# Optimization experiments

Measured on AMD Instinct MI355X. Metric: run time of the kernel, lower is better.

## Reference

```python
import jax, jax.numpy as jnp
import numpy as np

# Circuit structure constants (match init_kwargs)
N_NODES = 32768        # number of sum nodes in this layer
N_CHILD = 65536        # number of child nodes
NNZ = 1048576          # number of sparse weight entries (avg fan-in 32)
BATCH = 128


def setup_inputs() -> dict:
    key = jax.random.key(0)
    k1, k2, k3, k4 = jax.random.split(key, 4)
    # child log-likelihoods per sample (output of child layers)
    child_ll = jax.random.normal(k1, (BATCH, N_CHILD), dtype=jnp.float32)
    # sparse log-weights of the BCOO weight matrix [N_NODES, N_CHILD]
    log_w = jax.random.normal(k2, (NNZ,), dtype=jnp.float32)
    rows = jnp.sort(jax.random.randint(k3, (NNZ,), 0, N_NODES)).astype(jnp.int64)
    cols = jax.random.randint(k4, (NNZ,), 0, N_CHILD).astype(jnp.int64)
    return {"child_ll": child_ll, "log_w": log_w, "rows": rows, "cols": cols}


def reference(child_ll, log_w, rows, cols):
    """Faithful jax translation of SumLayer.log_likelihood_of_nodes.

    Original: per sample, exponentiate BCOO log-weights and child
    log-likelihoods, sparse matvec (weights @ exp(child_ll)), then
    log(result) - log_normalization_constants, where the normalization
    constants are log(row-sums of exp(log_weights)).
    """
    w = jnp.exp(log_w)  # [NNZ]
    # log normalization constants: log of row-sums of exp(log_weights)
    log_z = jnp.log(jax.ops.segment_sum(w, rows, num_segments=N_NODES))  # [N_NODES]

    def per_sample(ll):  # ll: [N_CHILD]
        p = jnp.exp(ll)
        contrib = w * p[cols]                                   # gather + weight [NNZ]
        return jax.ops.segment_sum(contrib, rows, num_segments=N_NODES)  # [N_NODES]

    s = jax.vmap(per_sample)(child_ll)  # [BATCH, N_NODES]
    return jnp.log(s) - log_z
```

## Files before the change

kernel.cpp:

```cpp
#include <hip/hip_runtime.h>
#include <math.h>

#define BATCH     128
#define N_NODES   32768
#define N_CHILD   65536
#define NNZ_TOTAL 1048576
#define LOG2E     1.44269504f

typedef __attribute__((ext_vector_type(2))) float fx2;

__global__ __launch_bounds__(256) void exp8_kernel(
    const float* __restrict__ child_ll, unsigned char* __restrict__ ex8,
    float* __restrict__ winv) {
    const int c0 = blockIdx.x * 64;
    const int t  = threadIdx.x;
    const int cl = t & 63;
    const int q  = t >> 6;

    float v[32];
    float m = -3.4e38f;
    const float* bp = child_ll + (size_t)(q * 32) * N_CHILD + c0 + cl;
#pragma unroll
    for (int j = 0; j < 32; ++j) {
        v[j] = bp[(size_t)j * N_CHILD];
        m = fmaxf(m, v[j]);
    }

    __shared__ float smx[4][64];
    __shared__ float skf[64];
    smx[q][cl] = m;
    __syncthreads();
    if (t < 64) {
        const float mm = fmaxf(fmaxf(smx[0][t], smx[1][t]),
                               fmaxf(smx[2][t], smx[3][t]));
        const int ks = 7 - (int)floorf(mm * LOG2E);
        skf[t] = (float)ks;
        winv[c0 + t] = exp2f((float)(-ks));
    }
    __syncthreads();
    const float kf = skf[cl];

    unsigned ow[8];
#pragma unroll
    for (int p = 0; p < 8; ++p) {
        const float a0 = exp2f(fmaf(v[4 * p + 0], LOG2E, kf));
        const float a1 = exp2f(fmaf(v[4 * p + 1], LOG2E, kf));
        const float a2 = exp2f(fmaf(v[4 * p + 2], LOG2E, kf));
        const float a3 = exp2f(fmaf(v[4 * p + 3], LOG2E, kf));
        unsigned u = 0;
        u = __builtin_amdgcn_cvt_pk_fp8_f32(a0, a1, u, false);
        u = __builtin_amdgcn_cvt_pk_fp8_f32(a2, a3, u, true);
        ow[p] = u;
    }

    __shared__ unsigned char sby[64 * 144];
    *(uint4*)&sby[cl * 144 + q * 32]      = *(uint4*)&ow[0];
    *(uint4*)&sby[cl * 144 + q * 32 + 16] = *(uint4*)&ow[4];
    __syncthreads();

    const int sub = t & 7, cc = t >> 3;
#pragma unroll
    for (int p = 0; p < 2; ++p) {
        const int c = cc + p * 32;
        *(uint4*)&ex8[(size_t)(c0 + c) * 128 + sub * 16] =
            *(const uint4*)&sby[c * 144 + sub * 16];
    }
}

__global__ __launch_bounds__(256) void fold_scan_kernel(
    const float* __restrict__ log_w, const int* __restrict__ cols,
    const float* __restrict__ winv, const int* __restrict__ rows,
    float* __restrict__ wfold, int* __restrict__ row_start) {
    const int i = (blockIdx.x * 256 + threadIdx.x) * 4;
    const float4 lw = *(const float4*)&log_w[i];
    const int4   cc = *(const int4*)&cols[i];
    float4 o;
    o.x = expf(lw.x) * winv[cc.x];
    o.y = expf(lw.y) * winv[cc.y];
    o.z = expf(lw.z) * winv[cc.z];
    o.w = expf(lw.w) * winv[cc.w];
    *(float4*)&wfold[i] = o;

    const int4 rv = *(const int4*)&rows[i];
    const int rj[4] = {rv.x, rv.y, rv.z, rv.w};
    int prev = (i == 0) ? -1 : rows[i - 1];
#pragma unroll
    for (int j = 0; j < 4; ++j) {
        const int cur = rj[j];
        if (cur != prev)
            for (int q = prev + 1; q <= cur; ++q) row_start[q] = i + j;
        prev = cur;
    }
    if (i + 3 == NNZ_TOTAL - 1)
        for (int q = rj[3] + 1; q <= N_NODES; ++q) row_start[q] = NNZ_TOTAL;
}

__global__ __launch_bounds__(256) void logz_kernel(
    const float* __restrict__ log_w, const int* __restrict__ row_start,
    float* __restrict__ logzv) {
    const int t = threadIdx.x;
    const int g = t >> 4, j = t & 15;
    const int r = blockIdx.x * 16 + g;
    const int s = row_start[r], e = row_start[r + 1];
    float sum = 0.f;
    for (int i = s + j; i < e; i += 16) sum += expf(log_w[i]);
    sum += __shfl_xor(sum, 1, 64);
    sum += __shfl_xor(sum, 2, 64);
    sum += __shfl_xor(sum, 4, 64);
    sum += __shfl_xor(sum, 8, 64);
    if (j == 0) logzv[r] = logf(sum);
}

__global__ __launch_bounds__(256, 4) void sum_rows_kernel(
    const unsigned char* __restrict__ ex8, const float* __restrict__ wfold,
    const int* __restrict__ cols, const int* __restrict__ row_start,
    const float* __restrict__ logzv, float* __restrict__ out) {
    const int wave = threadIdx.x >> 6;
    const int lane = threadIdx.x & 63;
    const int bid  = blockIdx.x;
    const int rb   = (bid & 7) * (N_NODES / 4 / 8) + (bid >> 3);
    const int r    = rb * 4 + wave;

    const int start = row_start[r];
    const int end   = row_start[r + 1];
    const int  slot = lane >> 3;
    const unsigned sub = (unsigned)lane & 7u;
    const unsigned boff = sub * 16u;

    float acc[16];
#pragma unroll
    for (int k = 0; k < 16; ++k) acc[k] = 0.f;

    for (int base = start; base < end; base += 64) {
        const int  idx   = base + lane;
        const bool valid = idx < end;
        const int   c  = __builtin_nontemporal_load(&cols[valid ? idx : start]);
        const float wf = valid ? __builtin_nontemporal_load(&wfold[idx]) : 0.f;
        const int seg = end - base;

        int   ct[8];
        float wt[8];
        uint4 g[8];

#pragma unroll
        for (int t8 = 0; t8 < 8; ++t8) {
            if (t8 * 8 < seg) {
                const int pa = (t8 * 8 + slot) * 4;
                ct[t8] = __builtin_amdgcn_ds_bpermute(pa, c);
                wt[t8] = __uint_as_float(__builtin_amdgcn_ds_bpermute(
                    pa, __float_as_uint(wf)));
            }
        }
#pragma unroll
        for (int t8 = 0; t8 < 8; ++t8) {
            if (t8 * 8 < seg)
                g[t8] = *(const uint4*)(ex8 +
                        ((size_t)(unsigned)ct[t8] << 7) + boff);
        }
#pragma unroll
        for (int t8 = 0; t8 < 8; ++t8) {
            if (t8 * 8 < seg) {
                const float wtv = wt[t8];
                const unsigned* gu = (const unsigned*)&g[t8];
#pragma unroll
                for (int q = 0; q < 4; ++q) {
                    const fx2 lo = __builtin_amdgcn_cvt_pk_f32_fp8((int)gu[q], false);
                    const fx2 hi = __builtin_amdgcn_cvt_pk_f32_fp8((int)gu[q], true);
                    acc[q * 4 + 0] = fmaf(wtv, lo.x, acc[q * 4 + 0]);
                    acc[q * 4 + 1] = fmaf(wtv, lo.y, acc[q * 4 + 1]);
                    acc[q * 4 + 2] = fmaf(wtv, hi.x, acc[q * 4 + 2]);
                    acc[q * 4 + 3] = fmaf(wtv, hi.y, acc[q * 4 + 3]);
                }
            }
        }
    }

#pragma unroll
    for (int k = 0; k < 16; ++k) {
        acc[k] += __shfl_xor(acc[k], 8, 64);
        acc[k] += __shfl_xor(acc[k], 16, 64);
        acc[k] += __shfl_xor(acc[k], 32, 64);
    }

    if (lane < 8) {
        const float lz = logzv[r];
        const int b0 = lane * 16;
#pragma unroll
        for (int k = 0; k < 16; ++k)
            out[(size_t)(b0 + k) * N_NODES + r] = logf(acc[k]) - lz;
    }
}

extern "C" void kernel_launch(void* const* d_in, const int* in_sizes, int n_in,
                              void* d_out, int out_size, void* d_ws, size_t ws_size,
                              hipStream_t stream) {
    const float* child_ll = (const float*)d_in[0];
    const float* log_w    = (const float*)d_in[1];
    const int*   rows     = (const int*)d_in[2];
    const int*   cols     = (const int*)d_in[3];
    float*       out      = (float*)d_out;

    unsigned char* ex8 = (unsigned char*)d_ws;
    float* winv      = (float*)((char*)d_ws + (size_t)N_CHILD * 128);
    float* wfold     = (float*)((char*)winv + (size_t)N_CHILD * 4);
    int*   row_start = (int*)((char*)wfold + (size_t)NNZ_TOTAL * 4);
    float* logzv     = (float*)((char*)row_start + (size_t)(N_NODES + 1) * 4);

    exp8_kernel<<<N_CHILD / 64, 256, 0, stream>>>(child_ll, ex8, winv);
    fold_scan_kernel<<<NNZ_TOTAL / 1024, 256, 0, stream>>>(
        log_w, cols, winv, rows, wfold, row_start);
    logz_kernel<<<N_NODES / 16, 256, 0, stream>>>(log_w, row_start, logzv);
    sum_rows_kernel<<<N_NODES / 4, 256, 0, stream>>>(ex8, wfold, cols,
                                                     row_start, logzv, out);
}
```

Baseline: 62.45 us.

## Fold row normalization sums into scan kernel via atomics and spread output stores

Removes the separate logz kernel. Row sums of exp(log_w) are now accumulated with atomicAdd in fold_scan_kernel, and the zeroing of those sums is folded into exp8_kernel. The final log and store in sum_rows_kernel are spread over all 64 lanes, each writing two outputs, instead of 8 lanes writing 16 each. This saves one launch and one reread of log_w, in exchange for atomic traffic and a float summation order that is no longer deterministic.

```diff
diff --git a/kernel.cpp b/kernel.cpp
--- a/kernel.cpp
+++ b/kernel.cpp
@@ -11,9 +11,12 @@
 
 __global__ __launch_bounds__(256) void exp8_kernel(
     const float* __restrict__ child_ll, unsigned char* __restrict__ ex8,
-    float* __restrict__ winv) {
+    float* __restrict__ winv, float* __restrict__ zsum) {
     const int c0 = blockIdx.x * 64;
     const int t  = threadIdx.x;
+    const int gid = blockIdx.x * 256 + t;
+    if (gid < N_NODES) zsum[gid] = 0.f;
+
     const int cl = t & 63;
     const int q  = t >> 6;
 
@@ -70,19 +73,32 @@
 __global__ __launch_bounds__(256) void fold_scan_kernel(
     const float* __restrict__ log_w, const int* __restrict__ cols,
     const float* __restrict__ winv, const int* __restrict__ rows,
-    float* __restrict__ wfold, int* __restrict__ row_start) {
+    float* __restrict__ wfold, int* __restrict__ row_start,
+    float* __restrict__ zsum) {
     const int i = (blockIdx.x * 256 + threadIdx.x) * 4;
     const float4 lw = *(const float4*)&log_w[i];
     const int4   cc = *(const int4*)&cols[i];
+    const float ew0 = expf(lw.x), ew1 = expf(lw.y);
+    const float ew2 = expf(lw.z), ew3 = expf(lw.w);
     float4 o;
-    o.x = expf(lw.x) * winv[cc.x];
-    o.y = expf(lw.y) * winv[cc.y];
-    o.z = expf(lw.z) * winv[cc.z];
-    o.w = expf(lw.w) * winv[cc.w];
+    o.x = ew0 * winv[cc.x];
+    o.y = ew1 * winv[cc.y];
+    o.z = ew2 * winv[cc.z];
+    o.w = ew3 * winv[cc.w];
     *(float4*)&wfold[i] = o;
 
     const int4 rv = *(const int4*)&rows[i];
     const int rj[4] = {rv.x, rv.y, rv.z, rv.w};
+    const float ej[4] = {ew0, ew1, ew2, ew3};
+
+    float s = ej[0];
+#pragma unroll
+    for (int j = 1; j < 4; ++j) {
+        if (rj[j] == rj[j - 1]) s += ej[j];
+        else { atomicAdd(&zsum[rj[j - 1]], s); s = ej[j]; }
+    }
+    atomicAdd(&zsum[rj[3]], s);
+
     int prev = (i == 0) ? -1 : rows[i - 1];
 #pragma unroll
     for (int j = 0; j < 4; ++j) {
@@ -95,26 +111,10 @@
         for (int q = rj[3] + 1; q <= N_NODES; ++q) row_start[q] = NNZ_TOTAL;
 }
 
-__global__ __launch_bounds__(256) void logz_kernel(
-    const float* __restrict__ log_w, const int* __restrict__ row_start,
-    float* __restrict__ logzv) {
-    const int t = threadIdx.x;
-    const int g = t >> 4, j = t & 15;
-    const int r = blockIdx.x * 16 + g;
-    const int s = row_start[r], e = row_start[r + 1];
-    float sum = 0.f;
-    for (int i = s + j; i < e; i += 16) sum += expf(log_w[i]);
-    sum += __shfl_xor(sum, 1, 64);
-    sum += __shfl_xor(sum, 2, 64);
-    sum += __shfl_xor(sum, 4, 64);
-    sum += __shfl_xor(sum, 8, 64);
-    if (j == 0) logzv[r] = logf(sum);
-}
-
 __global__ __launch_bounds__(256, 4) void sum_rows_kernel(
     const unsigned char* __restrict__ ex8, const float* __restrict__ wfold,
     const int* __restrict__ cols, const int* __restrict__ row_start,
-    const float* __restrict__ logzv, float* __restrict__ out) {
+    const float* __restrict__ zsum, float* __restrict__ out) {
     const int wave = threadIdx.x >> 6;
     const int lane = threadIdx.x & 63;
     const int bid  = blockIdx.x;
@@ -123,6 +123,7 @@
 
     const int start = row_start[r];
     const int end   = row_start[r + 1];
+    const float zs  = zsum[r];
     const int  slot = lane >> 3;
     const unsigned sub = (unsigned)lane & 7u;
     const unsigned boff = sub * 16u;
@@ -182,13 +183,17 @@
         acc[k] += __shfl_xor(acc[k], 32, 64);
     }
 
-    if (lane < 8) {
-        const float lz = logzv[r];
-        const int b0 = lane * 16;
-#pragma unroll
-        for (int k = 0; k < 16; ++k)
-            out[(size_t)(b0 + k) * N_NODES + r] = logf(acc[k]) - lz;
-    }
+    const float lz = logf(zs);
+    const int p  = lane >> 3;
+    const int b0 = (int)sub * 16 + 2 * p;
+    float v0 = acc[0], v1 = acc[1];
+#pragma unroll
+    for (int kk = 1; kk < 8; ++kk) {
+        v0 = (p == kk) ? acc[2 * kk]     : v0;
+        v1 = (p == kk) ? acc[2 * kk + 1] : v1;
+    }
+    out[(size_t)b0 * N_NODES + r]       = logf(v0) - lz;
+    out[(size_t)(b0 + 1) * N_NODES + r] = logf(v1) - lz;
 }
 
 extern "C" void kernel_launch(void* const* d_in, const int* in_sizes, int n_in,
@@ -204,12 +209,11 @@
     float* winv      = (float*)((char*)d_ws + (size_t)N_CHILD * 128);
     float* wfold     = (float*)((char*)winv + (size_t)N_CHILD * 4);
     int*   row_start = (int*)((char*)wfold + (size_t)NNZ_TOTAL * 4);
-    float* logzv     = (float*)((char*)row_start + (size_t)(N_NODES + 1) * 4);
-
-    exp8_kernel<<<N_CHILD / 64, 256, 0, stream>>>(child_ll, ex8, winv);
+    float* zsum      = (float*)((char*)row_start + (size_t)(N_NODES + 1) * 4);
+
+    exp8_kernel<<<N_CHILD / 64, 256, 0, stream>>>(child_ll, ex8, winv, zsum);
     fold_scan_kernel<<<NNZ_TOTAL / 1024, 256, 0, stream>>>(
-        log_w, cols, winv, rows, wfold, row_start);
-    logz_kernel<<<N_NODES / 16, 256, 0, stream>>>(log_w, row_start, logzv);
+        log_w, cols, winv, rows, wfold, row_start, zsum);
     sum_rows_kernel<<<N_NODES / 4, 256, 0, stream>>>(ex8, wfold, cols,
-                                                     row_start, logzv, out);
-}
+                                                     row_start, zsum, out);
+}
```

New measurement: 68.60 us. 1.1x slower.
